# Performance work log

Hardware: AMD Instinct MI355X
Metric: run time of the kernel (lower is better)

## Reference

```python
import jax, jax.numpy as jnp
import numpy as np
from jax import lax

B, L, T = 16, 400, 200
N_MELS, ENC, PRE = 80, 512, 256
QH, DH, ATTN = 1024, 1024, 128
NFILT, K = 32, 31
PAD = (K - 1) // 2  # 15


def setup_inputs() -> dict:
    key = jax.random.key(0)
    ks = jax.random.split(key, 20)
    def w(k, shape, s=0.05):
        return jax.random.normal(k, shape, dtype=jnp.float32) * s
    return {
        "memory": w(ks[0], (B, L, ENC), 1.0),
        "memory_lengths": jnp.full((B,), L, dtype=jnp.int32),
        "teacher": w(ks[1], (B, T, N_MELS), 1.0),
        # prenet (Linear bias=False x2)
        "pre_w1": w(ks[2], (PRE, N_MELS)),
        "pre_w2": w(ks[3], (PRE, PRE)),
        # query_rnn LSTMCell (input = prenet_dim + enc_embed_dim)
        "q_wih": w(ks[4], (4 * QH, PRE + ENC)),
        "q_whh": w(ks[5], (4 * QH, QH)),
        "q_bih": jnp.zeros((4 * QH,), jnp.float32),
        "q_bhh": jnp.zeros((4 * QH,), jnp.float32),
        # dec_rnn LSTMCell (input = query_rnn_dim + enc_embed_dim)
        "d_wih": w(ks[6], (4 * DH, QH + ENC)),
        "d_whh": w(ks[7], (4 * DH, DH)),
        "d_bih": jnp.zeros((4 * DH,), jnp.float32),
        "d_bhh": jnp.zeros((4 * DH,), jnp.float32),
        # location-sensitive attention
        "attn_wq": w(ks[8], (ATTN, QH)),
        "attn_wm": w(ks[9], (ATTN, ENC)),
        "attn_conv": w(ks[10], (NFILT, 2, K)),  # Conv1d(2 -> NFILT, k=31), bias=False
        "attn_wloc": w(ks[11], (ATTN, NFILT)),
        "attn_v": w(ks[12], (1, ATTN)),
        # output projections
        "proj_w": w(ks[13], (N_MELS, DH + ENC)),
        "proj_b": jnp.zeros((N_MELS,), jnp.float32),
        "gate_w": w(ks[14], (1, DH + ENC)),
        "gate_b": jnp.zeros((1,), jnp.float32),
    }


def _prenet(x, w1, w2):
    # dropout p=0 -> identity
    x = jax.nn.relu(x @ w1.T)
    return jax.nn.relu(x @ w2.T)


def _lstm_cell(x, h, c, wih, whh, bih, bhh):
    z = x @ wih.T + h @ whh.T + bih + bhh
    i, f, g, o = jnp.split(z, 4, axis=-1)  # torch LSTMCell gate order
    c = jax.nn.sigmoid(f) * c + jax.nn.sigmoid(i) * jnp.tanh(g)
    h = jax.nn.sigmoid(o) * jnp.tanh(c)
    return h, c


def reference(memory, memory_lengths, teacher, pre_w1, pre_w2,
              q_wih, q_whh, q_bih, q_bhh, d_wih, d_whh, d_bih, d_bhh,
              attn_wq, attn_wm, attn_conv, attn_wloc, attn_v,
              proj_w, proj_b, gate_w, gate_b):
    del memory_lengths  # forward() sets mask = None unconditionally
    processed_memory = memory @ attn_wm.T            # (B, L, ATTN)

    # teacher-forced prenet inputs (tf_rate=1.0, drop_dec_in=0.0)
    go = _prenet(jnp.zeros((B, N_MELS), memory.dtype), pre_w1, pre_w2)  # (B, PRE)
    tpre = _prenet(teacher, pre_w1, pre_w2)          # (B, T, PRE)
    dec_ins = jnp.concatenate([go[:, None], tpre[:, :-1]], axis=1)       # (B, T, PRE)
    dec_ins = dec_ins.transpose(1, 0, 2)             # (T, B, PRE)

    z = lambda *s: jnp.zeros(s, memory.dtype)
    carry0 = (z(B, QH), z(B, QH), z(B, DH), z(B, DH), z(B, L), z(B, L), z(B, ENC))

    def step(carry, dec_in):
        qh, qc, dh, dc, aw, aws, ctx = carry
        qh, qc = _lstm_cell(jnp.concatenate([dec_in, ctx], -1), qh, qc,
                            q_wih, q_whh, q_bih, q_bhh)
        # location-sensitive attention
        hist = jnp.stack([aw, aws], axis=1)          # (B, 2, L)
        loc = lax.conv_general_dilated(hist, attn_conv, (1,), [(PAD, PAD)],
                                       dimension_numbers=("NCH", "OIH", "NCH"))  # (B, NFILT, L)
        loc = jnp.einsum("bfl,af->bla", loc, attn_wloc)          # (B, L, ATTN)
        pq = (qh @ attn_wq.T)[:, None, :]                         # (B, 1, ATTN)
        energies = jnp.tanh(pq + loc + processed_memory) @ attn_v[0]  # (B, L)
        weights = jax.nn.softmax(energies, axis=-1)               # (B, L)
        ctx = jnp.einsum("bl,ble->be", weights, memory)           # (B, ENC)
        aws = aws + weights
        dh, dc = _lstm_cell(jnp.concatenate([ctx, qh], -1), dh, dc,
                            d_wih, d_whh, d_bih, d_bhh)
        feat = jnp.concatenate([dh, ctx], -1)                     # (B, DH+ENC)
        mel = feat @ proj_w.T + proj_b                            # (B, N_MELS)
        stop = jax.nn.sigmoid(feat @ gate_w.T + gate_b)[:, 0]     # (B,)
        return (qh, qc, dh, dc, weights, aws, ctx), (mel, weights, stop)

    _, (mels, aligns, stops) = lax.scan(step, carry0, dec_ins)
    mel_outputs = mels.transpose(1, 0, 2)      # (B, T, n_mels)  (n_frames_per_step=1)
    alignments = aligns.transpose(1, 0, 2)     # (B, T, L)
    stops = stops.transpose(1, 0)              # (B, T)
    return mel_outputs, alignments, stops
```

## Files before the change

### kernel.cpp

```cpp
#include <hip/hip_runtime.h>
#include <math.h>

#define Bsz 16
#define Lsz 400
#define Tsz 200
#define NMELS 80
#define ENC 512
#define PREsz 256
#define QHsz 1024
#define DHsz 1024
#define ATTNsz 128
#define NFILT 32
#define KW 31
#define PADW 15

typedef const float* __restrict__ cfp;
typedef float* __restrict__ fp;
typedef __fp16 hf;
typedef __fp16 h2 __attribute__((ext_vector_type(2)));
typedef const hf* __restrict__ chp;

union F4H { float4 f; h2 h[4]; };
union F2H4 { float2 f; hf h[4]; };

__device__ __forceinline__ float4 ldf4(const float* p){ return *reinterpret_cast<const float4*>(p); }
__device__ __forceinline__ float sigm(float x){ return 1.0f/(1.0f + __expf(-x)); }
__device__ __forceinline__ float tanhfast(float x){
  x = fminf(fmaxf(x, -15.0f), 15.0f);
  float e = __expf(2.0f*x);
  return (e-1.0f)/(e+1.0f);
}
__device__ __forceinline__ h2 pk2(float a, float b){
  return __builtin_amdgcn_cvt_pkrtz(a, b);
}
__device__ __forceinline__ float fdot2f(h2 a, h2 b, float c){
#if __has_builtin(__builtin_amdgcn_fdot2)
  return __builtin_amdgcn_fdot2(a, b, c, false);
#else
  return c + (float)a.x*(float)b.x + (float)a.y*(float)b.y;
#endif
}

__global__ void kzero(fp p, int n){
  int i = blockIdx.x*256 + threadIdx.x;
  if (i < n) p[i] = 0.0f;
}

__global__ void kcvt(cfp src, hf* __restrict__ dst, int n){
  int i = (blockIdx.x*256 + threadIdx.x)*4;
  if (i + 3 < n){
    float4 v = ldf4(src + i);
    dst[i+0] = (hf)v.x; dst[i+1] = (hf)v.y; dst[i+2] = (hf)v.z; dst[i+3] = (hf)v.w;
  } else {
    for (int k=i; k<n; k++) dst[k] = (hf)src[k];
  }
}

__global__ void kcvt_wq(cfp src, hf* __restrict__ dst){
  int idx = blockIdx.x*256 + threadIdx.x;
  int c = idx >> 8, rk = idx & 255;
  int r = rk >> 1, kh = rk & 1;
  const float* s = src + ((size_t)r*1024 + kh*512 + c*8);
  hf* d = dst + ((size_t)idx)*8;
  float4 v0 = ldf4(s), v1 = ldf4(s+4);
  d[0]=(hf)v0.x; d[1]=(hf)v0.y; d[2]=(hf)v0.z; d[3]=(hf)v0.w;
  d[4]=(hf)v1.x; d[5]=(hf)v1.y; d[6]=(hf)v1.z; d[7]=(hf)v1.w;
}

__global__ void __launch_bounds__(256) kprenet2(cfp teacher, cfp w1, cfp w2, fp dec_ins){
  int b = blockIdx.x & 15, tc = blockIdx.x >> 4;
  int t0 = tc*16;
  int tid = threadIdx.x;
  __shared__ __align__(16) float tch[16][80];
  __shared__ __align__(16) float h1[16][256];
  for (int idx = tid; idx < 16*80; idx += 256){
    int i = idx / 80, k = idx % 80;
    int t = t0 + i;
    float v = 0.f;
    if (t >= 1 && t < Tsz) v = teacher[((size_t)b*Tsz + (t-1))*NMELS + k];
    tch[i][k] = v;
  }
  __syncthreads();
  {
    int r = tid;
    float acc[16];
    #pragma unroll
    for (int i=0;i<16;i++) acc[i]=0.f;
    const float* wr = w1 + (size_t)r*80;
    for (int k=0;k<80;k++){
      float w = wr[k];
      #pragma unroll
      for (int i=0;i<16;i++) acc[i] += w * tch[i][k];
    }
    #pragma unroll
    for (int i=0;i<16;i++) h1[i][r] = fmaxf(acc[i], 0.f);
  }
  __syncthreads();
  {
    int r = tid;
    float acc[16];
    #pragma unroll
    for (int i=0;i<16;i++) acc[i]=0.f;
    const float* wr = w2 + (size_t)r*256;
    for (int k=0;k<256;k++){
      float w = wr[k];
      #pragma unroll
      for (int i=0;i<16;i++) acc[i] += w * h1[i][k];
    }
    for (int i=0;i<16;i++){
      int t = t0 + i;
      if (t < Tsz){
        float v = (t == 0) ? 0.f : fmaxf(acc[i], 0.f);
        dec_ins[((size_t)t*Bsz + b)*PREsz + r] = v;
      }
    }
  }
}

__global__ void __launch_bounds__(256) kpm2(cfp memory, cfp wm, fp pm){
  int b = blockIdx.x / 25, lc = blockIdx.x % 25;
  int l0 = lc*16;
  int tid = threadIdx.x;
  __shared__ __align__(16) float mrow[16][512];
  {
    const float4* s4 = (const float4*)(memory + ((size_t)b*Lsz + l0)*ENC);
    float4* d4 = (float4*)&mrow[0][0];
    #pragma unroll
    for (int i=0;i<8;i++) d4[tid + i*256] = s4[tid + i*256];
  }
  __syncthreads();
  int a = tid & 127, g = tid >> 7;
  const float* wr = wm + (size_t)a*ENC;
  float acc[8];
  #pragma unroll
  for (int i=0;i<8;i++) acc[i]=0.f;
  for (int k=0;k<512;k+=4){
    float4 w4 = ldf4(wr + k);
    #pragma unroll
    for (int i=0;i<8;i++){
      float4 x4 = ldf4(&mrow[g*8+i][k]);
      acc[i] += w4.x*x4.x + w4.y*x4.y + w4.z*x4.z + w4.w*x4.w;
    }
  }
  #pragma unroll
  for (int i=0;i<8;i++)
    pm[((size_t)b*Lsz + l0 + g*8 + i)*ATTNsz + a] = acc[i];
}

struct GateSmem { __align__(16) h2 xsh[16][132]; };
struct ConvSmem { float hists[2][80]; float convo[NFILT][50]; float cwsh[NFILT*2*KW]; float stat2[2]; };
union SMemA { GateSmem g; ConvSmem c; };
struct MidQSmem {
  __align__(16) h2 qh2l[512];
  float pqv[128], vsh[128];
  float esh[100], pesh[100];
  float red4[4], red4b[4];
  __align__(16) float4 psum[128];
};
struct MidDSmem { __align__(16) h2 feath[768]; float scs[4]; };
union SMemB { MidQSmem q; MidDSmem d; };

__device__ __forceinline__ void gatesA_item(
    int w, int t, int do_q, int do_d, SMemA& sm, int tid,
    cfp dec_ins, cfp qh_state, cfp dh_state,
    cfp cpartP, cfp emaxP, cfp esumP, cfp ebufP,
    cfp awsP, fp awsQ,
    fp qpart, fp dpart, fp loc, fp out_align,
    chp h_qwih, chp h_qwhh, chp h_dwih, chp h_dwhh,
    cfp conv_w, cfp wloc, cfp pm)
{
  if (w >= 144){
    int gid = w - 144;
    int isq = (gid < 224);
    if (isq ? !do_q : !do_d) return;
    int idx = isq ? gid : (gid - 224);
    int nch = isq ? 7 : 10;
    int c = idx % nch, rg = idx / nch;
    int bb = tid >> 4, quar = tid & 15;
    int is_ctx = isq ? (c >= 1 && c <= 2) : (c <= 1);
    int ctxoff = isq ? (c-1)*256 : c*256;
    h2* dst = &sm.g.xsh[bb][quar*8];
    if (is_ctx){
      if (!do_d){
        h2 z = pk2(0.f, 0.f);
        #pragma unroll
        for (int i=0;i<8;i++) dst[i] = z;
      } else {
        float m0=emaxP[bb*4+0], m1=emaxP[bb*4+1], m2=emaxP[bb*4+2], m3=emaxP[bb*4+3];
        float gm = fmaxf(fmaxf(m0,m1), fmaxf(m2,m3));
        float e0=__expf(m0-gm), e1=__expf(m1-gm), e2=__expf(m2-gm), e3=__expf(m3-gm);
        float gs = esumP[bb*4+0]*e0 + esumP[bb*4+1]*e1 + esumP[bb*4+2]*e2 + esumP[bb*4+3]*e3;
        float inv = 1.0f/gs;
        float s0=e0*inv, s1=e1*inv, s2=e2*inv, s3=e3*inv;
        const float* cp = cpartP + (size_t)bb*2048 + ctxoff + quar*16;
        #pragma unroll
        for (int kk=0;kk<16;kk+=4){
          float4 p0 = ldf4(cp+kk), p1 = ldf4(cp+512+kk), p2 = ldf4(cp+1024+kk), p3 = ldf4(cp+1536+kk);
          float ax = s0*p0.x + s1*p1.x + s2*p2.x + s3*p3.x;
          float ay = s0*p0.y + s1*p1.y + s2*p2.y + s3*p3.y;
          float az = s0*p0.z + s1*p1.z + s2*p2.z + s3*p3.z;
          float aw = s0*p0.w + s1*p1.w + s2*p2.w + s3*p3.w;
          dst[(kk>>1)+0] = pk2(ax, ay);
          dst[(kk>>1)+1] = pk2(az, aw);
        }
      }
    } else {
      const float* src;
      if (isq){
        if (c == 0)      src = dec_ins + (size_t)t*Bsz*PREsz + bb*PREsz;
        else             src = qh_state + bb*QHsz + (c-3)*256;
      } else {
        if (c < 6)       src = qh_state + bb*QHsz + (c-2)*256;
        else             src = dh_state + bb*DHsz + (c-6)*256;
      }
      const float4* s4 = (const float4*)(src + quar*16);
      float4 t0=s4[0], t1=s4[1], t2=s4[2], t3=s4[3];
      dst[0]=pk2(t0.x,t0.y); dst[1]=pk2(t0.z,t0.w);
      dst[2]=pk2(t1.x,t1.y); dst[3]=pk2(t1.z,t1.w);
      dst[4]=pk2(t2.x,t2.y); dst[5]=pk2(t2.z,t2.w);
      dst[6]=pk2(t3.x,t3.y); dst[7]=pk2(t3.z,t3.w);
    }
    __syncthreads();
    int b = tid & 15, rl = tid >> 4;
    int row0 = rg*128 + rl*8;
    const hf* wbase; int wstride, woff;
    if (isq){
      if (c < 3){ wbase = h_qwih; wstride = 768;  woff = c*256; }
      else      { wbase = h_qwhh; wstride = 1024; woff = (c-3)*256; }
    } else {
      if (c < 6){ wbase = h_dwih; wstride = 1536; woff = c*256; }
      else      { wbase = h_dwhh; wstride = 1024; woff = (c-6)*256; }
    }
    const h2* xr = &sm.g.xsh[b][0];
    float acc[8];
    #pragma unroll
    for (int r=0;r<8;r++) acc[r]=0.f;
    #pragma unroll 1
    for (int kb=0; kb<128; kb+=8){
      F4H xA, xB;
      xA.f = ldf4((const float*)(xr + kb));
      xB.f = ldf4((const float*)(xr + kb + 4));
      #pragma unroll
      for (int r=0;r<8;r+=2){
        const h2* wa = (const h2*)(wbase + (size_t)(row0+r)*wstride + woff);
        const h2* wb = (const h2*)(wbase + (size_t)(row0+r+1)*wstride + woff);
        F4H u0, u1, u2, u3;
        u0.f = ldf4((const float*)(wa + kb));
        u1.f = ldf4((const float*)(wa + kb + 4));
        u2.f = ldf4((const float*)(wb + kb));
        u3.f = ldf4((const float*)(wb + kb + 4));
        #pragma unroll
        for (int j=0;j<4;j++){
          acc[r]   = fdot2f(u0.h[j], xA.h[j], acc[r]);
          acc[r]   = fdot2f(u1.h[j], xB.h[j], acc[r]);
          acc[r+1] = fdot2f(u2.h[j], xA.h[j], acc[r+1]);
          acc[r+1] = fdot2f(u3.h[j], xB.h[j], acc[r+1]);
        }
      }
    }
    fp part = isq ? qpart : dpart;
    float4 o0 = {acc[0], acc[1], acc[2], acc[3]};
    float4 o1 = {acc[4], acc[5], acc[6], acc[7]};
    *reinterpret_cast<float4*>(part + ((size_t)(c*16 + b))*4096 + row0) = o0;
    *reinterpret_cast<float4*>(part + ((size_t)(c*16 + b))*4096 + row0 + 4) = o1;
  } else if (w < 128){
    if (!do_q) return;
    int b = w >> 3, chunk = w & 7;
    int l0 = chunk*50;
    for (int i=tid; i<NFILT*2*KW; i+=256) sm.c.cwsh[i] = conv_w[i];
    if (tid == 0 && do_d){
      float m0=emaxP[b*4+0], m1=emaxP[b*4+1], m2=emaxP[b*4+2], m3=emaxP[b*4+3];
      float gm = fmaxf(fmaxf(m0,m1), fmaxf(m2,m3));
      float gs = esumP[b*4+0]*__expf(m0-gm) + esumP[b*4+1]*__expf(m1-gm)
               + esumP[b*4+2]*__expf(m2-gm) + esumP[b*4+3]*__expf(m3-gm);
      sm.c.stat2[0] = gm; sm.c.stat2[1] = 1.0f/gs;
    }
    __syncthreads();
    float gm = sm.c.stat2[0], ginv = sm.c.stat2[1];
    for (int i=tid; i<80; i+=256){
      int pos = l0 - PADW + i;
      float w2 = 0.f, as = 0.f;
      if (do_d && pos >= 0 && pos < Lsz){
        w2 = __expf(ebufP[b*Lsz + pos] - gm) * ginv;
        as = awsP[b*Lsz + pos] + w2;
      }
      sm.c.hists[0][i] = w2;
      sm.c.hists[1][i] = as;
    }
    __syncthreads();
    for (int task=tid; task<NFILT*50; task+=256){
      int f = task & 31, ll = task >> 5;
      float a = 0.0f;
      const float* c0 = &sm.c.cwsh[(f*2+0)*KW];
      const float* c1 = &sm.c.cwsh[(f*2+1)*KW];
      #pragma unroll
      for (int k=0;k<KW;k++) a += sm.c.hists[0][ll+k]*c0[k] + sm.c.hists[1][ll+k]*c1[k];
      sm.c.convo[f][ll] = a;
    }
    __syncthreads();
    for (int task=tid; task<50*ATTNsz; task+=256){
      int a = task & 127, ll = task >> 7;
      float s = 0.0f;
      const float* wl = wloc + a*NFILT;
      #pragma unroll
      for (int f=0;f<NFILT;f++) s += sm.c.convo[f][ll]*wl[f];
      size_t gi = ((size_t)b*Lsz + l0 + ll)*ATTNsz + a;
      loc[gi] = s + pm[gi];
    }
  } else {
    if (!do_d) return;
    int b = w - 128;
    if (tid == 0){
      float m0=emaxP[b*4+0], m1=emaxP[b*4+1], m2=emaxP[b*4+2], m3=emaxP[b*4+3];
      float gm = fmaxf(fmaxf(m0,m1), fmaxf(m2,m3));
      float gs = esumP[b*4+0]*__expf(m0-gm) + esumP[b*4+1]*__expf(m1-gm)
               + esumP[b*4+2]*__expf(m2-gm) + esumP[b*4+3]*__expf(m3-gm);
      sm.c.stat2[0] = gm; sm.c.stat2[1] = 1.0f/gs;
    }
    __syncthreads();
    float gm = sm.c.stat2[0], ginv = sm.c.stat2[1];
    for (int l=tid; l<Lsz; l+=256){
      float w2 = __expf(ebufP[b*Lsz + l] - gm) * ginv;
      awsQ[b*Lsz + l] = awsP[b*Lsz + l] + w2;
      out_align[((size_t)b*Tsz + (t-1))*Lsz + l] = w2;
    }
  }
}

__device__ __forceinline__ void midB_qitem(
    int w, int t, MidQSmem& S, int tid,
    cfp qpart, cfp qcP, fp qcQ, fp qh_state,
    chp h_wq, cfp vvec, cfp loc, chp h_mem,
    fp cpartQ, fp emaxQ, fp esumQ, fp ebufQ,
    cfp q_bih, cfp q_bhh)
{
  int b = w & 15, lc = w >> 4;
  int l0 = lc*100;
  int lane = tid & 63, wv = tid >> 6;
  {
    int j4 = tid*4;
    float4 acc[4];
    #pragma unroll
    for (int g=0; g<4; g++){
      int r4 = g*1024 + j4;
      float4 bi = ldf4(q_bih + r4), bh = ldf4(q_bhh + r4);
      float4 a = {bi.x+bh.x, bi.y+bh.y, bi.z+bh.z, bi.w+bh.w};
      #pragma unroll
      for (int c=0;c<7;c++){
        float4 p = ldf4(qpart + ((size_t)(c*16 + b))*4096 + r4);
        a.x += p.x; a.y += p.y; a.z += p.z; a.w += p.w;
      }
      acc[g] = a;
    }
    float4 zi = acc[0], zf = acc[1], zg = acc[2], zo = acc[3];
    float4 cp = ldf4(qcP + b*QHsz + j4);
    float4 cn, hn;
    cn.x = sigm(zf.x)*cp.x + sigm(zi.x)*tanhfast(zg.x); hn.x = sigm(zo.x)*tanhfast(cn.x);
    cn.y = sigm(zf.y)*cp.y + sigm(zi.y)*tanhfast(zg.y); hn.y = sigm(zo.y)*tanhfast(cn.y);
    cn.z = sigm(zf.z)*cp.z + sigm(zi.z)*tanhfast(zg.z); hn.z = sigm(zo.z)*tanhfast(cn.z);
    cn.w = sigm(zf.w)*cp.w + sigm(zi.w)*tanhfast(zg.w); hn.w = sigm(zo.w)*tanhfast(cn.w);
    if (lc == 0){
      *reinterpret_cast<float4*>(qcQ + b*QHsz + j4) = cn;
      *reinterpret_cast<float4*>(qh_state + b*QHsz + j4) = hn;
    }
    S.qh2l[tid*2+0] = pk2(hn.x, hn.y);
    S.qh2l[tid*2+1] = pk2(hn.z, hn.w);
  }
  if (tid < 128) S.vsh[tid] = vvec[tid];
  __syncthreads();
  {
    int kh = tid & 1;
    const h2* wq2 = (const h2*)h_wq;
    const h2* xr = &S.qh2l[kh*256];
    int l4 = tid*4;
    float acc = 0.f;
    #pragma unroll 4
    for (int c=0;c<64;c+=2){
      F4H wA, wB, xA, xB;
      wA.f = ldf4((const float*)(wq2 + c*1024 + l4));
      wB.f = ldf4((const float*)(wq2 + (c+1)*1024 + l4));
      xA.f = ldf4((const float*)(xr + c*4));
      xB.f = ldf4((const float*)(xr + c*4 + 4));
      #pragma unroll
      for (int j=0;j<4;j++){
        acc = fdot2f(wA.h[j], xA.h[j], acc);
        acc = fdot2f(wB.h[j], xB.h[j], acc);
      }
    }
    acc += __shfl_xor(acc, 1, 64);
    if (kh == 0) S.pqv[tid >> 1] = acc;
  }
  __syncthreads();
  {
    int ll = tid >> 1, ah = tid & 1;
    float e = 0.f;
    if (ll < 100){
      int l = l0 + ll;
      const float* lp = loc + ((size_t)b*Lsz + l)*ATTNsz + ah*64;
      const float* pqa = &S.pqv[ah*64];
      const float* va  = &S.vsh[ah*64];
      #pragma unroll 4
      for (int a=0;a<64;a+=4){
        float4 l4 = ldf4(lp+a);
        e += tanhfast(pqa[a+0]+l4.x)*va[a+0];
        e += tanhfast(pqa[a+1]+l4.y)*va[a+1];
        e += tanhfast(pqa[a+2]+l4.z)*va[a+2];
        e += tanhfast(pqa[a+3]+l4.w)*va[a+3];
      }
    }
    e += __shfl_xor(e, 1, 64);
    if (ll < 100 && ah == 0) S.esh[ll] = e;
  }
  __syncthreads();
  {
    float lm = (tid < 100) ? S.esh[tid] : -1e30f;
    #pragma unroll
    for (int off=32; off>0; off>>=1) lm = fmaxf(lm, __shfl_xor(lm, off, 64));
    if (lane == 0) S.red4[wv] = lm;
    __syncthreads();
    float mx = fmaxf(fmaxf(S.red4[0], S.red4[1]), fmaxf(S.red4[2], S.red4[3]));
    float p = 0.f;
    if (tid < 100){
      p = __expf(S.esh[tid]-mx);
      S.pesh[tid] = p;
      ebufQ[b*Lsz + l0 + tid] = S.esh[tid];
    }
    float ls = p;
    #pragma unroll
    for (int off=32; off>0; off>>=1) ls += __shfl_xor(ls, off, 64);
    if (lane == 0) S.red4b[wv] = ls;
    __syncthreads();
    if (tid == 0){
      emaxQ[b*4+lc] = mx;
      esumQ[b*4+lc] = S.red4b[0]+S.red4b[1]+S.red4b[2]+S.red4b[3];
    }
  }
  {
    int e4 = tid & 127, lh = tid >> 7;
    const hf* mp = h_mem + ((size_t)b*Lsz + l0)*ENC + e4*4;
    float4 a = {0.f,0.f,0.f,0.f};
    for (int l = lh*50; l < lh*50+50; l++){
      float w2 = S.pesh[l];
      F2H4 m; m.f = *reinterpret_cast<const float2*>(mp + (size_t)l*ENC);
      a.x += w2*(float)m.h[0]; a.y += w2*(float)m.h[1];
      a.z += w2*(float)m.h[2]; a.w += w2*(float)m.h[3];
    }
    if (lh == 1) S.psum[e4] = a;
    __syncthreads();
    if (lh == 0){
      float4 p = S.psum[e4];
      a.x += p.x; a.y += p.y; a.z += p.z; a.w += p.w;
      *reinterpret_cast<float4*>(cpartQ + ((size_t)b*4 + lc)*512 + e4*4) = a;
    }
  }
}

__device__ __forceinline__ void midB_ditem(
    int w, int t, MidDSmem& S, int tid,
    cfp dpart, cfp dcP, fp dcQ, fp dh_state,
    cfp cpartP, cfp emaxP, cfp esumP,
    cfp d_bih, cfp d_bhh,
    chp h_proj, cfp proj_b, chp h_gate, cfp gate_b,
    fp out_mel, fp out_stop)
{
  int db = w - 64;
  int b = db & 15, half = db >> 4;
  int tm = t - 1;
  int lane = tid & 63, wv = tid >> 6;
  {
    int j4 = tid*4;
    float4 acc[4];
    #pragma unroll
    for (int g=0; g<4; g++){
      int r4 = g*1024 + j4;
      float4 bi = ldf4(d_bih + r4), bh = ldf4(d_bhh + r4);
      float4 a = {bi.x+bh.x, bi.y+bh.y, bi.z+bh.z, bi.w+bh.w};
      #pragma unroll
      for (int c=0;c<10;c++){
        float4 p = ldf4(dpart + ((size_t)(c*16 + b))*4096 + r4);
        a.x += p.x; a.y += p.y; a.z += p.z; a.w += p.w;
      }
      acc[g] = a;
    }
    if (tid == 0){
      float m0=emaxP[b*4+0], m1=emaxP[b*4+1], m2=emaxP[b*4+2], m3=emaxP[b*4+3];
      float gm = fmaxf(fmaxf(m0,m1), fmaxf(m2,m3));
      float e0=__expf(m0-gm), e1=__expf(m1-gm), e2=__expf(m2-gm), e3=__expf(m3-gm);
      float gs = esumP[b*4+0]*e0 + esumP[b*4+1]*e1 + esumP[b*4+2]*e2 + esumP[b*4+3]*e3;
      float inv = 1.0f/gs;
      S.scs[0]=e0*inv; S.scs[1]=e1*inv; S.scs[2]=e2*inv; S.scs[3]=e3*inv;
    }
    float4 zi = acc[0], zf = acc[1], zg = acc[2], zo = acc[3];
    float4 cp = ldf4(dcP + b*DHsz + j4);
    float4 cn, hn;
    cn.x = sigm(zf.x)*cp.x + sigm(zi.x)*tanhfast(zg.x); hn.x = sigm(zo.x)*tanhfast(cn.x);
    cn.y = sigm(zf.y)*cp.y + sigm(zi.y)*tanhfast(zg.y); hn.y = sigm(zo.y)*tanhfast(cn.y);
    cn.z = sigm(zf.z)*cp.z + sigm(zi.z)*tanhfast(zg.z); hn.z = sigm(zo.z)*tanhfast(cn.z);
    cn.w = sigm(zf.w)*cp.w + sigm(zi.w)*tanhfast(zg.w); hn.w = sigm(zo.w)*tanhfast(cn.w);
    if (half == 0){
      *reinterpret_cast<float4*>(dcQ + b*DHsz + j4) = cn;
      *reinterpret_cast<float4*>(dh_state + b*DHsz + j4) = hn;
    }
    S.feath[tid*2+0] = pk2(hn.x, hn.y);
    S.feath[tid*2+1] = pk2(hn.z, hn.w);
  }
  __syncthreads();
  {
    float s0=S.scs[0], s1=S.scs[1], s2=S.scs[2], s3=S.scs[3];
    int i0 = tid*2;
    const float* cp = cpartP + (size_t)b*2048;
    float v0 = s0*cp[i0]   + s1*cp[512+i0]   + s2*cp[1024+i0]   + s3*cp[1536+i0];
    float v1 = s0*cp[i0+1] + s1*cp[512+i0+1] + s2*cp[1024+i0+1] + s3*cp[1536+i0+1];
    S.feath[512 + tid] = pk2(v0, v1);
  }
  __syncthreads();
  int rbeg = half*40, rend = half ? 81 : 40;
  for (int r = rbeg + wv; r < rend; r += 4){
    const h2* wr = (r < 80) ? (const h2*)(h_proj + (size_t)r*1536) : (const h2*)h_gate;
    float acc = 0.0f;
    #pragma unroll
    for (int m=0;m<3;m++){
      int k4 = (lane + 64*m)*4;
      F4H wt, x;
      wt.f = ldf4((const float*)(wr + k4));
      x.f = ldf4((const float*)(&S.feath[k4]));
      #pragma unroll
      for (int j=0;j<4;j++) acc = fdot2f(wt.h[j], x.h[j], acc);
    }
    #pragma unroll
    for (int off=32; off>0; off>>=1) acc += __shfl_xor(acc, off, 64);
    if (lane == 0){
      if (r < 80) out_mel[((size_t)b*Tsz + tm)*NMELS + r] = acc + proj_b[r];
      else        out_stop[b*Tsz + tm] = sigm(acc + gate_b[0]);
    }
  }
}

struct KParams {
  const float* dec_ins;
  float* pm; float* loc;
  float* qpart; float* dpart;
  float* ebuf2; float* emax2; float* esum2; float* cpart2;
  float* qh_state; float* dh_state; float* qc2; float* dc2; float* aws2;
  const hf* h_qwih; const hf* h_qwhh; const hf* h_dwih; const hf* h_dwhh;
  const hf* h_wq; const hf* h_proj; const hf* h_gate; const hf* h_mem;
  const float* conv_w; const float* wloc; const float* vvec;
  const float* q_bih; const float* q_bhh; const float* d_bih; const float* d_bhh;
  const float* proj_b; const float* gate_b;
  float* out_mel; float* out_align; float* out_stop;
};

__global__ void __launch_bounds__(256) kgatesL(int t, KParams P)
{
  int pp = (t+1)&1, qq = t&1;
  int do_q = (t < Tsz) ? 1 : 0;
  int do_d = (t > 0) ? 1 : 0;
  __shared__ SMemA sm;
  gatesA_item(blockIdx.x, t, do_q, do_d, sm, threadIdx.x,
    P.dec_ins, P.qh_state, P.dh_state,
    P.cpart2 + pp*32768, P.emax2 + pp*64, P.esum2 + pp*64, P.ebuf2 + pp*6400,
    P.aws2 + pp*6400, P.aws2 + qq*6400,
    P.qpart, P.dpart, P.loc, P.out_align,
    P.h_qwih, P.h_qwhh, P.h_dwih, P.h_dwhh,
    P.conv_w, P.wloc, P.pm);
}

__global__ void __launch_bounds__(256) kmidL(int t, KParams P)
{
  int pp = (t+1)&1, qq = t&1;
  int do_q = (t < Tsz) ? 1 : 0;
  int do_d = (t > 0) ? 1 : 0;
  __shared__ SMemB sm;
  int w = blockIdx.x;
  if (w < 64){
    if (do_q)
      midB_qitem(w, t, sm.q, threadIdx.x,
        P.qpart, P.qc2 + pp*16384, P.qc2 + qq*16384, P.qh_state,
        P.h_wq, P.vvec, P.loc, P.h_mem,
        P.cpart2 + qq*32768, P.emax2 + qq*64, P.esum2 + qq*64, P.ebuf2 + qq*6400,
        P.q_bih, P.q_bhh);
  } else {
    if (do_d)
      midB_ditem(w, t, sm.d, threadIdx.x,
        P.dpart, P.dc2 + pp*16384, P.dc2 + qq*16384, P.dh_state,
        P.cpart2 + pp*32768, P.emax2 + pp*64, P.esum2 + pp*64,
        P.d_bih, P.d_bhh,
        P.h_proj, P.proj_b, P.h_gate, P.gate_b,
        P.out_mel, P.out_stop);
  }
}

extern "C" void kernel_launch(void* const* d_in, const int* in_sizes, int n_in,
                              void* d_out, int out_size, void* d_ws, size_t ws_size,
                              hipStream_t stream)
{
  const float* memory  = (const float*)d_in[0];
  const float* teacher = (const float*)d_in[2];
  const float* pre_w1  = (const float*)d_in[3];
  const float* pre_w2  = (const float*)d_in[4];
  const float* q_wih   = (const float*)d_in[5];
  const float* q_whh   = (const float*)d_in[6];
  const float* q_bih   = (const float*)d_in[7];
  const float* q_bhh   = (const float*)d_in[8];
  const float* d_wih   = (const float*)d_in[9];
  const float* d_whh   = (const float*)d_in[10];
  const float* d_bih   = (const float*)d_in[11];
  const float* d_bhh   = (const float*)d_in[12];
  const float* attn_wq   = (const float*)d_in[13];
  const float* attn_wm   = (const float*)d_in[14];
  const float* attn_conv = (const float*)d_in[15];
  const float* attn_wloc = (const float*)d_in[16];
  const float* attn_v    = (const float*)d_in[17];
  const float* proj_w  = (const float*)d_in[18];
  const float* proj_b  = (const float*)d_in[19];
  const float* gate_w  = (const float*)d_in[20];
  const float* gate_b  = (const float*)d_in[21];

  float* ws = (float*)d_ws;
  float* dec_ins  = ws;
  float* pm       = dec_ins + 819200;
  float* loc      = pm + 819200;
  float* qpart    = loc + 819200;
  float* dpart    = qpart + 458752;
  float* ebuf2    = dpart + 655360;
  float* emax2    = ebuf2 + 12800;
  float* esum2    = emax2 + 128;
  float* cpart2   = esum2 + 128;
  float* qh_state = cpart2 + 65536;
  float* dh_state = qh_state + 16384;
  float* qc2      = dh_state + 16384;
  float* dc2      = qc2 + 32768;
  float* aws2     = dc2 + 32768;
  float* fend     = aws2 + 12800;

  hf* h_qwih = (hf*)fend;
  hf* h_qwhh = h_qwih + 3145728;
  hf* h_dwih = h_qwhh + 4194304;
  hf* h_dwhh = h_dwih + 6291456;
  hf* h_wq   = h_dwhh + 4194304;
  hf* h_proj = h_wq + 131072;
  hf* h_gate = h_proj + 122880;
  hf* h_mem  = h_gate + 1536;

  float* out_mel   = (float*)d_out;
  float* out_align = out_mel + (size_t)Bsz*Tsz*NMELS;
  float* out_stop  = out_align + (size_t)Bsz*Tsz*Lsz;

  const int stateN = 16384+16384+32768+32768+12800;
  kzero<<<dim3((stateN+255)/256), dim3(256), 0, stream>>>(qh_state, stateN);
  kcvt<<<dim3(3145728/1024), dim3(256), 0, stream>>>(q_wih, h_qwih, 3145728);
  kcvt<<<dim3(4194304/1024), dim3(256), 0, stream>>>(q_whh, h_qwhh, 4194304);
  kcvt<<<dim3(6291456/1024), dim3(256), 0, stream>>>(d_wih, h_dwih, 6291456);
  kcvt<<<dim3(4194304/1024), dim3(256), 0, stream>>>(d_whh, h_dwhh, 4194304);
  kcvt_wq<<<dim3(64), dim3(256), 0, stream>>>(attn_wq, h_wq);
  kcvt<<<dim3(122880/1024), dim3(256), 0, stream>>>(proj_w, h_proj, 122880);
  kcvt<<<dim3(2), dim3(256), 0, stream>>>(gate_w, h_gate, 1536);
  kcvt<<<dim3(3276800/1024), dim3(256), 0, stream>>>(memory, h_mem, 3276800);
  kprenet2<<<dim3(16*13), dim3(256), 0, stream>>>(teacher, pre_w1, pre_w2, dec_ins);
  kpm2<<<dim3(400), dim3(256), 0, stream>>>(memory, attn_wm, pm);

  KParams P;
  P.dec_ins = dec_ins; P.pm = pm; P.loc = loc;
  P.qpart = qpart; P.dpart = dpart;
  P.ebuf2 = ebuf2; P.emax2 = emax2; P.esum2 = esum2; P.cpart2 = cpart2;
  P.qh_state = qh_state; P.dh_state = dh_state;
  P.qc2 = qc2; P.dc2 = dc2; P.aws2 = aws2;
  P.h_qwih = h_qwih; P.h_qwhh = h_qwhh; P.h_dwih = h_dwih; P.h_dwhh = h_dwhh;
  P.h_wq = h_wq; P.h_proj = h_proj; P.h_gate = h_gate; P.h_mem = h_mem;
  P.conv_w = attn_conv; P.wloc = attn_wloc; P.vvec = attn_v;
  P.q_bih = q_bih; P.q_bhh = q_bhh; P.d_bih = d_bih; P.d_bhh = d_bhh;
  P.proj_b = proj_b; P.gate_b = gate_b;
  P.out_mel = out_mel; P.out_align = out_align; P.out_stop = out_stop;

  for (int t = 0; t <= Tsz; t++){
    kgatesL<<<dim3(688), dim3(256), 0, stream>>>(t, P);
    kmidL<<<dim3(96), dim3(256), 0, stream>>>(t, P);
  }
}
```

Measured before the change: 8.641 ms.

## Fuse per-step gate and mid kernels with in-kernel atomic flag synchronization

Merges the two kernels launched per timestep into one kernel of 784 blocks. The first 96 blocks run the attention/LSTM-update work of the previous step and then bump a global counter. The remaining blocks wait on that counter before running the gate matvecs for the current step. This halves the number of launches and removes one launch gap per step. In exchange, gate blocks busy-wait, and correctness relies on all blocks being co-resident, so a scheduling order where waiting blocks starve the producers would deadlock.

```diff
diff --git a/kernel.cpp b/kernel.cpp
--- a/kernel.cpp
+++ b/kernel.cpp
@@ -159,6 +159,7 @@
 };
 struct MidDSmem { __align__(16) h2 feath[768]; float scs[4]; };
 union SMemB { MidQSmem q; MidDSmem d; };
+union SMemAll { SMemA a; SMemB b; };
 
 __device__ __forceinline__ void gatesA_item(
     int w, int t, int do_q, int do_d, SMemA& sm, int tid,
@@ -550,43 +551,69 @@
   float* out_mel; float* out_align; float* out_stop;
 };
 
-__global__ void __launch_bounds__(256) kgatesL(int t, KParams P)
+__global__ void __launch_bounds__(256, 4) kfused(int t, unsigned target, unsigned* __restrict__ flag, KParams P)
 {
-  int pp = (t+1)&1, qq = t&1;
-  int do_q = (t < Tsz) ? 1 : 0;
-  int do_d = (t > 0) ? 1 : 0;
-  __shared__ SMemA sm;
-  gatesA_item(blockIdx.x, t, do_q, do_d, sm, threadIdx.x,
-    P.dec_ins, P.qh_state, P.dh_state,
-    P.cpart2 + pp*32768, P.emax2 + pp*64, P.esum2 + pp*64, P.ebuf2 + pp*6400,
-    P.aws2 + pp*6400, P.aws2 + qq*6400,
-    P.qpart, P.dpart, P.loc, P.out_align,
-    P.h_qwih, P.h_qwhh, P.h_dwih, P.h_dwhh,
-    P.conv_w, P.wloc, P.pm);
-}
-
-__global__ void __launch_bounds__(256) kmidL(int t, KParams P)
-{
-  int pp = (t+1)&1, qq = t&1;
-  int do_q = (t < Tsz) ? 1 : 0;
-  int do_d = (t > 0) ? 1 : 0;
-  __shared__ SMemB sm;
-  int w = blockIdx.x;
-  if (w < 64){
-    if (do_q)
-      midB_qitem(w, t, sm.q, threadIdx.x,
-        P.qpart, P.qc2 + pp*16384, P.qc2 + qq*16384, P.qh_state,
-        P.h_wq, P.vvec, P.loc, P.h_mem,
-        P.cpart2 + qq*32768, P.emax2 + qq*64, P.esum2 + qq*64, P.ebuf2 + qq*6400,
-        P.q_bih, P.q_bhh);
+  int bid = blockIdx.x, tid = threadIdx.x;
+  __shared__ SMemAll sm;
+  if (bid < 96){
+    int tmid = t - 1;
+    if (tmid >= 0){
+      int pp = (tmid+1)&1, qq = tmid&1;
+      int do_q = (tmid < Tsz) ? 1 : 0;
+      int do_d = (tmid > 0) ? 1 : 0;
+      int w = bid;
+      if (w < 64){
+        if (do_q)
+          midB_qitem(w, tmid, sm.b.q, tid,
+            P.qpart, P.qc2 + pp*16384, P.qc2 + qq*16384, P.qh_state,
+            P.h_wq, P.vvec, P.loc, P.h_mem,
+            P.cpart2 + qq*32768, P.emax2 + qq*64, P.esum2 + qq*64, P.ebuf2 + qq*6400,
+            P.q_bih, P.q_bhh);
+      } else {
+        if (do_d)
+          midB_ditem(w, tmid, sm.b.d, tid,
+            P.dpart, P.dc2 + pp*16384, P.dc2 + qq*16384, P.dh_state,
+            P.cpart2 + pp*32768, P.emax2 + pp*64, P.esum2 + pp*64,
+            P.d_bih, P.d_bhh,
+            P.h_proj, P.proj_b, P.h_gate, P.gate_b,
+            P.out_mel, P.out_stop);
+      }
+    }
+    __syncthreads();
+    if (tid == 0){
+      __threadfence();
+      atomicAdd(flag, 1u);
+    }
   } else {
-    if (do_d)
-      midB_ditem(w, t, sm.d, threadIdx.x,
-        P.dpart, P.dc2 + pp*16384, P.dc2 + qq*16384, P.dh_state,
-        P.cpart2 + pp*32768, P.emax2 + pp*64, P.esum2 + pp*64,
-        P.d_bih, P.d_bhh,
-        P.h_proj, P.proj_b, P.h_gate, P.gate_b,
-        P.out_mel, P.out_stop);
+    int w = bid - 96;
+    int do_q = (t < Tsz) ? 1 : 0;
+    int do_d = (t > 0 && t <= Tsz) ? 1 : 0;
+    int active;
+    if (w >= 144)      active = (w - 144 < 224) ? do_q : do_d;
+    else if (w < 128)  active = do_q;
+    else               active = do_d;
+    if (!active) return;
+    if (target){
+      if (tid == 0){
+#if __has_builtin(__hip_atomic_load)
+        while (__hip_atomic_load(flag, __ATOMIC_RELAXED, __HIP_MEMORY_SCOPE_AGENT) < target)
+          __builtin_amdgcn_s_sleep(1);
+        (void)__hip_atomic_load(flag, __ATOMIC_ACQUIRE, __HIP_MEMORY_SCOPE_AGENT);
+#else
+        while (atomicAdd(flag, 0u) < target) __builtin_amdgcn_s_sleep(1);
+        __threadfence();
+#endif
+      }
+      __syncthreads();
+    }
+    int pp = (t+1)&1, qq = t&1;
+    gatesA_item(w, t, do_q, do_d, sm.a, tid,
+      P.dec_ins, P.qh_state, P.dh_state,
+      P.cpart2 + pp*32768, P.emax2 + pp*64, P.esum2 + pp*64, P.ebuf2 + pp*6400,
+      P.aws2 + pp*6400, P.aws2 + qq*6400,
+      P.qpart, P.dpart, P.loc, P.out_align,
+      P.h_qwih, P.h_qwhh, P.h_dwih, P.h_dwhh,
+      P.conv_w, P.wloc, P.pm);
   }
 }
 
@@ -641,6 +668,7 @@
   hf* h_proj = h_wq + 131072;
   hf* h_gate = h_proj + 122880;
   hf* h_mem  = h_gate + 1536;
+  unsigned* syncflag = (unsigned*)(h_mem + 3276800);
 
   float* out_mel   = (float*)d_out;
   float* out_align = out_mel + (size_t)Bsz*Tsz*NMELS;
@@ -648,6 +676,7 @@
 
   const int stateN = 16384+16384+32768+32768+12800;
   kzero<<<dim3((stateN+255)/256), dim3(256), 0, stream>>>(qh_state, stateN);
+  kzero<<<dim3(1), dim3(256), 0, stream>>>((float*)syncflag, 1);
   kcvt<<<dim3(3145728/1024), dim3(256), 0, stream>>>(q_wih, h_qwih, 3145728);
   kcvt<<<dim3(4194304/1024), dim3(256), 0, stream>>>(q_whh, h_qwhh, 4194304);
   kcvt<<<dim3(6291456/1024), dim3(256), 0, stream>>>(d_wih, h_dwih, 6291456);
@@ -672,8 +701,8 @@
   P.proj_b = proj_b; P.gate_b = gate_b;
   P.out_mel = out_mel; P.out_align = out_align; P.out_stop = out_stop;
 
-  for (int t = 0; t <= Tsz; t++){
-    kgatesL<<<dim3(688), dim3(256), 0, stream>>>(t, P);
-    kmidL<<<dim3(96), dim3(256), 0, stream>>>(t, P);
-  }
-}
+  for (int t = 0; t <= Tsz + 1; t++){
+    unsigned target = 96u * (unsigned)(t + 1);
+    kfused<<<dim3(784), dim3(256), 0, stream>>>(t, target, syncflag, P);
+  }
+}
```

Result: slower. 13.40 ms (+55.1%).
